# Kernel tuning notes

Measured on AMD Instinct MI355X. Metric: run time of the kernel, lower is better.

Reference implementation:

```python
import jax, jax.numpy as jnp
import numpy as np

N = 50000      # nodes
E = 800000     # random edges (self-loops added in reference, per PyG GATConv default)
F_IN = 128
B = 512        # graphs in the batch
NEG_SLOPE = 0.2  # PyG GATConv leaky_relu default


def setup_inputs() -> dict:
    key = jax.random.key(0)
    ks = jax.random.split(key, 12)
    def w(k, shape, fan_in):
        return jax.random.normal(k, shape, jnp.float32) / np.sqrt(fan_in)
    return {
        "x": jax.random.normal(ks[0], (N, F_IN), jnp.float32),
        "edge_index": jax.random.randint(ks[1], (2, E), 0, N, dtype=jnp.int32),
        "batch": jnp.sort(jax.random.randint(ks[2], (N,), 0, B, dtype=jnp.int32)),
        "W1": w(ks[3], (F_IN, 4 * 64), F_IN),
        "a_src1": w(ks[4], (4, 64), 64),
        "a_dst1": w(ks[5], (4, 64), 64),
        "b1": jnp.zeros((4 * 64,), jnp.float32),
        "W2": w(ks[6], (256, 1 * 128), 256),
        "a_src2": w(ks[7], (1, 128), 128),
        "a_dst2": w(ks[8], (1, 128), 128),
        "b2": jnp.zeros((128,), jnp.float32),
        "Wl": w(ks[9], (128, 1), 128),
        "bl": jnp.zeros((1,), jnp.float32),
    }


def gat_layer(x, src, dst, W, a_src, a_dst, b, n):
    H, Fo = a_src.shape
    h = (x @ W).reshape(n, H, Fo)                      # [N,H,Fo]
    alpha_s = jnp.einsum("nhf,hf->nh", h, a_src)       # [N,H]
    alpha_d = jnp.einsum("nhf,hf->nh", h, a_dst)
    e = jax.nn.leaky_relu(alpha_s[src] + alpha_d[dst], NEG_SLOPE)  # [E,H]
    # segment softmax over incoming edges of each dst node
    m = jax.ops.segment_max(e, dst, num_segments=n)    # [N,H]; self-loops => every node hit
    ex = jnp.exp(e - m[dst])
    den = jax.ops.segment_sum(ex, dst, num_segments=n)
    alpha = ex / den[dst]                              # [E,H]
    out = jax.ops.segment_sum(h[src] * alpha[:, :, None], dst, num_segments=n)
    return out.reshape(n, H * Fo) + b


def reference(x, edge_index, batch, W1, a_src1, a_dst1, b1, W2, a_src2, a_dst2, b2, Wl, bl):
    n = x.shape[0]
    loops = jnp.arange(n, dtype=edge_index.dtype)
    src = jnp.concatenate([edge_index[0], loops])
    dst = jnp.concatenate([edge_index[1], loops])
    h = jax.nn.elu(gat_layer(x, src, dst, W1, a_src1, a_dst1, b1, n))
    h = jax.nn.elu(gat_layer(h, src, dst, W2, a_src2, a_dst2, b2, n))
    # dropout omitted (inference)
    sums = jax.ops.segment_sum(h, batch, num_segments=B)
    cnt = jax.ops.segment_sum(jnp.ones((n,), h.dtype), batch, num_segments=B)
    g = sums / jnp.maximum(cnt, 1.0)[:, None]          # global_mean_pool -> [B,128]
    return jax.nn.sigmoid(g @ Wl + bl).reshape(-1)     # [B]
```

## Files before the change

### kernel.cpp

```cpp
#include <hip/hip_runtime.h>
#include <hip/hip_bf16.h>

#define NN 50000
#define EE 800000
#define ETOT 850000
#define BB 512
#define CAP 64
#define SCAT_BLKS ((ETOT + 255) / 256)

typedef __hip_bfloat16 bf16;
typedef __attribute__((ext_vector_type(8))) __bf16 v8bf;
typedef __attribute__((ext_vector_type(4))) float f32x4;

__device__ __forceinline__ float lo2f(unsigned int u) {
    return __uint_as_float(u << 16);
}
__device__ __forceinline__ float hi2f(unsigned int u) {
    return __uint_as_float(u & 0xffff0000u);
}
__device__ __forceinline__ float us2f(unsigned short u) {
    return __uint_as_float(((unsigned int)u) << 16);
}
__device__ __forceinline__ unsigned short f2bfbits(float f) {
    bf16 h = __float2bfloat16(f);
    return *reinterpret_cast<unsigned short*>(&h);
}
__device__ __forceinline__ float lrelu_exp(float ev) {
    ev = ev > 0.f ? ev : 0.2f * ev;
    return __expf(fminf(ev, 80.f));
}

__global__ void k_prep(const float* __restrict__ W1, const float* __restrict__ W2,
                       bf16* __restrict__ wt1, bf16* __restrict__ wt2,
                       int* __restrict__ deg, float* __restrict__ gsum) {
    int idx = blockIdx.x * blockDim.x + threadIdx.x;
    if (idx < 256 * 128) {
        int c = idx >> 7, k = idx & 127;
        wt1[idx] = __float2bfloat16(W1[k * 256 + c]);
    } else {
        int j = idx - 256 * 128;
        int c = j >> 8, k = j & 255;
        wt2[j] = __float2bfloat16(W2[k * 128 + c]);
    }
    if (idx < NN) deg[idx] = 0;
    gsum[idx] = 0.f;
}

__global__ __launch_bounds__(256, 2)
void k_scatter_gemm1(const int* __restrict__ srcArr, const int* __restrict__ dstArr,
                     int* __restrict__ deg, unsigned short* __restrict__ csrc,
                     const float* __restrict__ x, const bf16* __restrict__ wt1,
                     const float* __restrict__ aw_s, const float* __restrict__ aw_d,
                     bf16* __restrict__ h1, float* __restrict__ as1,
                     float* __restrict__ ad1) {
    __shared__ bf16 xs[32 * 136];
    if (blockIdx.x < SCAT_BLKS) {
        int e = blockIdx.x * 256 + threadIdx.x;
        if (e < ETOT) {
            int d, s;
            if (e < EE) { d = dstArr[e]; s = srcArr[e]; }
            else        { d = e - EE;    s = d; }
            d = min(max(d, 0), NN - 1);
            s = min(max(s, 0), NN - 1);
            int p = atomicAdd(&deg[d], 1);
            if (p < CAP) csrc[d * CAP + p] = (unsigned short)s;
        }
        return;
    }

    int bid = blockIdx.x - SCAT_BLKS;
    int n0 = bid * 32;
    int t = threadIdx.x;
    for (int i = 0; i < 4; i++) {
        int idx = t + 256 * i;
        int r = idx >> 5, c4 = idx & 31;
        float4 v = make_float4(0.f, 0.f, 0.f, 0.f);
        if (n0 + r < NN) v = *(const float4*)(x + (size_t)(n0 + r) * 128 + c4 * 4);
        ushort4 o;
        o.x = f2bfbits(v.x); o.y = f2bfbits(v.y);
        o.z = f2bfbits(v.z); o.w = f2bfbits(v.w);
        *(ushort4*)(&xs[r * 136 + c4 * 4]) = o;
    }
    __syncthreads();

    int wv = t >> 6, lane = t & 63;
    int q = lane >> 4, r16 = lane & 15;
    int rowBase = (wv & 1) * 16;
    int colBase = (wv >> 1) * 128;

    f32x4 acc[8];
#pragma unroll
    for (int ct = 0; ct < 8; ct++) acc[ct] = (f32x4){0.f, 0.f, 0.f, 0.f};

#pragma unroll
    for (int kt = 0; kt < 4; kt++) {
        v8bf va = *(const v8bf*)(&xs[(rowBase + r16) * 136 + kt * 32 + q * 8]);
#pragma unroll
        for (int ct = 0; ct < 8; ct++) {
            v8bf vb = *(const v8bf*)(wt1 + (size_t)(colBase + ct * 16 + r16) * 128 + kt * 32 + q * 8);
            acc[ct] = __builtin_amdgcn_mfma_f32_16x16x32_bf16(va, vb, acc[ct], 0, 0, 0);
        }
    }

    float wsv[8], wdv[8];
#pragma unroll
    for (int ct = 0; ct < 8; ct++) {
        int col = colBase + ct * 16 + r16;
        wsv[ct] = aw_s[col];
        wdv[ct] = aw_d[col];
    }

    float ps[4][2], pd[4][2];
#pragma unroll
    for (int reg = 0; reg < 4; reg++) {
        ps[reg][0] = 0.f; ps[reg][1] = 0.f;
        pd[reg][0] = 0.f; pd[reg][1] = 0.f;
    }

#pragma unroll
    for (int reg = 0; reg < 4; reg++) {
        int node = n0 + rowBase + q * 4 + reg;
        bool ok = node < NN;
#pragma unroll
        for (int ct = 0; ct < 8; ct++) {
            float v = acc[ct][reg];
            if (ok) h1[(size_t)node * 256 + colBase + ct * 16 + r16] = __float2bfloat16(v);
            ps[reg][ct >> 2] += v * wsv[ct];
            pd[reg][ct >> 2] += v * wdv[ct];
        }
    }

#pragma unroll
    for (int reg = 0; reg < 4; reg++) {
        int node = n0 + rowBase + q * 4 + reg;
        bool ok = node < NN;
#pragma unroll
        for (int lh = 0; lh < 2; lh++) {
            float a = ps[reg][lh], b = pd[reg][lh];
            for (int mask = 1; mask <= 8; mask <<= 1) {
                a += __shfl_xor(a, mask);
                b += __shfl_xor(b, mask);
            }
            if (r16 == 0 && ok) {
                int head = (wv >> 1) * 2 + lh;
                as1[node * 4 + head] = a;
                ad1[node * 4 + head] = b;
            }
        }
    }
}

__global__ void k_gather1(const unsigned short* __restrict__ csrc, const int* __restrict__ deg,
                          const bf16* __restrict__ h1, const float* __restrict__ as1,
                          const float* __restrict__ ad1, const float* __restrict__ b1,
                          bf16* __restrict__ x2) {
    int bid = blockIdx.x;
    int n = bid >> 1, slice = bid & 1;
    int t = threadIdx.x;
    int lh = t >> 5;
    int cnt = min(deg[n], CAP);
    float2 ad = *(const float2*)&ad1[n * 4 + slice * 2];
    __shared__ unsigned int ls[CAP];
    __shared__ float la[CAP * 2];
    const char* h1c = (const char*)h1;
    unsigned int tconst = (unsigned int)(slice * 128 + t * 2) * 2;
    if (t < cnt) {
        int s = (int)csrc[n * CAP + t];
        ls[t] = (unsigned int)s << 9;
        float2 as = *(const float2*)&as1[s * 4 + slice * 2];
        la[t * 2 + 0] = lrelu_exp(as.x + ad.x);
        la[t * 2 + 1] = lrelu_exp(as.y + ad.y);
    }
    __syncthreads();
    float a0 = 0.f, a1 = 0.f, ssum = 0.f;
    int j = 0;
    for (; j + 3 < cnt; j += 4) {
        unsigned int o0 = ls[j] + tconst, o1 = ls[j + 1] + tconst;
        unsigned int o2 = ls[j + 2] + tconst, o3 = ls[j + 3] + tconst;
        float A0 = la[j * 2 + lh], A1 = la[j * 2 + 2 + lh];
        float A2 = la[j * 2 + 4 + lh], A3 = la[j * 2 + 6 + lh];
        unsigned int u0 = *(const unsigned int*)(h1c + o0);
        unsigned int u1 = *(const unsigned int*)(h1c + o1);
        unsigned int u2 = *(const unsigned int*)(h1c + o2);
        unsigned int u3 = *(const unsigned int*)(h1c + o3);
        ssum += (A0 + A1) + (A2 + A3);
        a0 = fmaf(A0, lo2f(u0), a0); a0 = fmaf(A1, lo2f(u1), a0);
        a0 = fmaf(A2, lo2f(u2), a0); a0 = fmaf(A3, lo2f(u3), a0);
        a1 = fmaf(A0, hi2f(u0), a1); a1 = fmaf(A1, hi2f(u1), a1);
        a1 = fmaf(A2, hi2f(u2), a1); a1 = fmaf(A3, hi2f(u3), a1);
    }
    for (; j < cnt; j++) {
        unsigned int o0 = ls[j] + tconst;
        float A0 = la[j * 2 + lh];
        unsigned int u0 = *(const unsigned int*)(h1c + o0);
        ssum += A0;
        a0 = fmaf(A0, lo2f(u0), a0);
        a1 = fmaf(A0, hi2f(u0), a1);
    }
    float inv = 1.f / fmaxf(ssum, 1e-35f);
    int c = slice * 128 + t * 2;
    float r0 = a0 * inv + b1[c + 0];
    float r1 = a1 * inv + b1[c + 1];
    r0 = r0 > 0.f ? r0 : (__expf(r0) - 1.f);
    r1 = r1 > 0.f ? r1 : (__expf(r1) - 1.f);
    unsigned int packed = (unsigned int)f2bfbits(r0) | ((unsigned int)f2bfbits(r1) << 16);
    *(unsigned int*)((unsigned short*)x2 + (size_t)n * 256 + c) = packed;
}

__global__ __launch_bounds__(256, 2)
void k_gemm2(const bf16* __restrict__ x2, const bf16* __restrict__ wt2,
             const float* __restrict__ aw_s, const float* __restrict__ aw_d,
             bf16* __restrict__ h2, float* __restrict__ as2,
             float* __restrict__ ad2) {
    int n0 = blockIdx.x * 32;
    int t = threadIdx.x;
    __shared__ bf16 xs[32 * 264];
    __shared__ float psPart[32][2];
    __shared__ float pdPart[32][2];
    for (int i = 0; i < 4; i++) {
        int idx = t + 256 * i;
        int r = idx >> 5, c8 = idx & 31;
        uint4 v;
        if (n0 + r < NN) v = *(const uint4*)(x2 + (size_t)(n0 + r) * 256 + c8 * 8);
        else             v = make_uint4(0, 0, 0, 0);
        *(uint4*)(&xs[r * 264 + c8 * 8]) = v;
    }
    __syncthreads();

    int wv = t >> 6, lane = t & 63;
    int q = lane >> 4, r16 = lane & 15;
    int rowBase = (wv & 1) * 16;
    int colBase = (wv >> 1) * 64;

    f32x4 acc[4];
#pragma unroll
    for (int ct = 0; ct < 4; ct++) acc[ct] = (f32x4){0.f, 0.f, 0.f, 0.f};

#pragma unroll
    for (int kt = 0; kt < 8; kt++) {
        v8bf va = *(const v8bf*)(&xs[(rowBase + r16) * 264 + kt * 32 + q * 8]);
#pragma unroll
        for (int ct = 0; ct < 4; ct++) {
            v8bf vb = *(const v8bf*)(wt2 + (size_t)(colBase + ct * 16 + r16) * 256 + kt * 32 + q * 8);
            acc[ct] = __builtin_amdgcn_mfma_f32_16x16x32_bf16(va, vb, acc[ct], 0, 0, 0);
        }
    }

    float wsv[4], wdv[4];
#pragma unroll
    for (int ct = 0; ct < 4; ct++) {
        int col = colBase + ct * 16 + r16;
        wsv[ct] = aw_s[col];
        wdv[ct] = aw_d[col];
    }

#pragma unroll
    for (int reg = 0; reg < 4; reg++) {
        int node = n0 + rowBase + q * 4 + reg;
        bool ok = node < NN;
        float ps = 0.f, pd = 0.f;
#pragma unroll
        for (int ct = 0; ct < 4; ct++) {
            float v = acc[ct][reg];
            if (ok) h2[(size_t)node * 128 + colBase + ct * 16 + r16] = __float2bfloat16(v);
            ps += v * wsv[ct];
            pd += v * wdv[ct];
        }
        for (int mask = 1; mask <= 8; mask <<= 1) {
            ps += __shfl_xor(ps, mask);
            pd += __shfl_xor(pd, mask);
        }
        if (r16 == 0) {
            int li = rowBase + q * 4 + reg;
            psPart[li][wv >> 1] = ps;
            pdPart[li][wv >> 1] = pd;
        }
    }
    __syncthreads();
    if (t < 32) {
        int node = n0 + t;
        if (node < NN) {
            as2[node] = psPart[t][0] + psPart[t][1];
            ad2[node] = pdPart[t][0] + pdPart[t][1];
        }
    }
}

__global__ __launch_bounds__(512, 2)
void k_gather2pool(const unsigned short* __restrict__ csrc, const int* __restrict__ deg,
                   const bf16* __restrict__ h2, const float* __restrict__ as2,
                   const float* __restrict__ ad2, const float* __restrict__ b2,
                   const int* __restrict__ batch, float* __restrict__ gsum) {
    int wv = threadIdx.x >> 6;
    int t = threadIdx.x & 63;
    int n = blockIdx.x * 8 + wv;
    int cnt = min(deg[n], CAP);
    float adn = ad2[n];
    __shared__ unsigned int ls[8][CAP];
    __shared__ float la[8][CAP];
    __shared__ float acc[8][128];
    const char* h2c = (const char*)h2;
    unsigned int tconst = (unsigned int)t * 4;
    if (t < cnt) {
        int s = (int)csrc[n * CAP + t];
        ls[wv][t] = (unsigned int)s << 8;
        la[wv][t] = lrelu_exp(as2[s] + adn);
    }
    __syncthreads();
    const unsigned int* lsw = ls[wv];
    const float* law = la[wv];
    float a0 = 0.f, a1 = 0.f, ssum = 0.f;
    int j = 0;
    for (; j + 3 < cnt; j += 4) {
        unsigned int o0 = lsw[j] + tconst, o1 = lsw[j + 1] + tconst;
        unsigned int o2 = lsw[j + 2] + tconst, o3 = lsw[j + 3] + tconst;
        float A0 = law[j], A1 = law[j + 1], A2 = law[j + 2], A3 = law[j + 3];
        unsigned int u0 = *(const unsigned int*)(h2c + o0);
        unsigned int u1 = *(const unsigned int*)(h2c + o1);
        unsigned int u2 = *(const unsigned int*)(h2c + o2);
        unsigned int u3 = *(const unsigned int*)(h2c + o3);
        ssum += (A0 + A1) + (A2 + A3);
        a0 = fmaf(A0, lo2f(u0), a0); a0 = fmaf(A1, lo2f(u1), a0);
        a0 = fmaf(A2, lo2f(u2), a0); a0 = fmaf(A3, lo2f(u3), a0);
        a1 = fmaf(A0, hi2f(u0), a1); a1 = fmaf(A1, hi2f(u1), a1);
        a1 = fmaf(A2, hi2f(u2), a1); a1 = fmaf(A3, hi2f(u3), a1);
    }
    for (; j < cnt; j++) {
        unsigned int o0 = lsw[j] + tconst;
        float A0 = law[j];
        unsigned int u0 = *(const unsigned int*)(h2c + o0);
        ssum += A0;
        a0 = fmaf(A0, lo2f(u0), a0);
        a1 = fmaf(A0, hi2f(u0), a1);
    }
    float inv = 1.f / fmaxf(ssum, 1e-35f);
    int c = t * 2;
    float r0 = a0 * inv + b2[c + 0];
    float r1 = a1 * inv + b2[c + 1];
    r0 = r0 > 0.f ? r0 : (__expf(r0) - 1.f);
    r1 = r1 > 0.f ? r1 : (__expf(r1) - 1.f);
    acc[wv][c] = r0;
    acc[wv][c + 1] = r1;
    __syncthreads();
    int tt = threadIdx.x;
    if (tt < 128) {
        int n0 = blockIdx.x * 8;
        int b0 = batch[n0], b7 = batch[n0 + 7];
        if (b0 == b7) {
            float s = 0.f;
#pragma unroll
            for (int w = 0; w < 8; w++) s += acc[w][tt];
            atomicAdd(&gsum[b0 * 128 + tt], s);
        } else {
#pragma unroll
            for (int w = 0; w < 8; w++)
                atomicAdd(&gsum[batch[n0 + w] * 128 + tt], acc[w][tt]);
        }
    }
}

__global__ void k_out(const float* __restrict__ gsum, const int* __restrict__ batch,
                      const float* __restrict__ Wl, const float* __restrict__ bl,
                      float* __restrict__ out) {
    int b = blockIdx.x;
    int t = threadIdx.x;
    int lo = 0, hi = NN;
    while (lo < hi) { int m = (lo + hi) >> 1; if (batch[m] < b) lo = m + 1; else hi = m; }
    int start = lo;
    int lo2 = start, hi2 = NN;
    while (lo2 < hi2) { int m = (lo2 + hi2) >> 1; if (batch[m] < b + 1) lo2 = m + 1; else hi2 = m; }
    int cnt = lo2 - start;
    float g = gsum[b * 128 + t] / (float)(cnt > 0 ? cnt : 1);
    float p = g * Wl[t];
    for (int o = 32; o > 0; o >>= 1) p += __shfl_down(p, o);
    __shared__ float red[2];
    if ((t & 63) == 0) red[t >> 6] = p;
    __syncthreads();
    if (t == 0) {
        float acc = red[0] + red[1] + bl[0];
        out[b] = 1.f / (1.f + __expf(-acc));
    }
}

extern "C" void kernel_launch(void* const* d_in, const int* in_sizes, int n_in,
                              void* d_out, int out_size, void* d_ws, size_t ws_size,
                              hipStream_t stream) {
    const float* x = (const float*)d_in[0];
    const int* ei = (const int*)d_in[1];
    const int* batch = (const int*)d_in[2];
    const float* W1 = (const float*)d_in[3];
    const float* aw_s1 = (const float*)d_in[4];
    const float* aw_d1 = (const float*)d_in[5];
    const float* b1 = (const float*)d_in[6];
    const float* W2 = (const float*)d_in[7];
    const float* aw_s2 = (const float*)d_in[8];
    const float* aw_d2 = (const float*)d_in[9];
    const float* b2 = (const float*)d_in[10];
    const float* Wl = (const float*)d_in[11];
    const float* bl = (const float*)d_in[12];
    const int* srcArr = ei;
    const int* dstArr = ei + EE;

    char* w = (char*)d_ws;
    size_t off = 0;
    auto alloc = [&](size_t bytes) -> void* {
        void* p = (void*)(w + off);
        off = (off + bytes + 255) & ~(size_t)255;
        return p;
    };
    bf16* bufA = (bf16*)alloc((size_t)NN * 256 * 2);
    bf16* bufB = (bf16*)alloc((size_t)NN * 256 * 2);
    unsigned short* csrc = (unsigned short*)alloc((size_t)NN * CAP * 2);
    float* as1 = (float*)alloc((size_t)NN * 4 * 4);
    float* ad1 = (float*)alloc((size_t)NN * 4 * 4);
    float* as2 = (float*)alloc((size_t)NN * 4);
    float* ad2 = (float*)alloc((size_t)NN * 4);
    int* deg = (int*)alloc((size_t)NN * 4);
    float* gsum = (float*)alloc((size_t)BB * 128 * 4);
    bf16* wt1 = (bf16*)alloc((size_t)256 * 128 * 2);
    bf16* wt2 = (bf16*)alloc((size_t)128 * 256 * 2);
    (void)ws_size;

    k_prep<<<256, 256, 0, stream>>>(W1, W2, wt1, wt2, deg, gsum);

    bf16* h1 = bufA;
    bf16* x2 = bufB;
    int gemmBlocks = (NN + 31) / 32;
    k_scatter_gemm1<<<SCAT_BLKS + gemmBlocks, 256, 0, stream>>>(
        srcArr, dstArr, deg, csrc, x, wt1, aw_s1, aw_d1, h1, as1, ad1);

    k_gather1<<<NN * 2, 64, 0, stream>>>(csrc, deg, h1, as1, ad1, b1, x2);

    bf16* h2 = bufA;
    k_gemm2<<<gemmBlocks, 256, 0, stream>>>(x2, wt2, aw_s2, aw_d2, h2, as2, ad2);

    k_gather2pool<<<NN / 8, 512, 0, stream>>>(csrc, deg, h2, as2, ad2, b2, batch, gsum);

    k_out<<<BB, 128, 0, stream>>>(gsum, batch, Wl, bl, (float*)d_out);
}
```

Baseline: 310.0 us.

## Build compact CSR adjacency via count, scan and place instead of padded slots

Replaces the fixed-capacity padded per-node neighbor table with a compact CSR layout. The first kernel now only counts in-degrees, with self-loops seeded by initialising the counts to one. A single-block scan then computes offsets and places each node's self-loop, and a placement kernel scatters the edge sources through atomic cursors. The gather kernels read contiguous neighbor lists, shrinking the adjacency footprint, at the cost of two extra launches and a serial single-block scan.

```diff
diff --git a/kernel.cpp b/kernel.cpp
--- a/kernel.cpp
+++ b/kernel.cpp
@@ -3,14 +3,14 @@
 
 #define NN 50000
 #define EE 800000
-#define ETOT 850000
 #define BB 512
 #define CAP 64
-#define SCAT_BLKS ((ETOT + 255) / 256)
 
 typedef __hip_bfloat16 bf16;
 typedef __attribute__((ext_vector_type(8))) __bf16 v8bf;
 typedef __attribute__((ext_vector_type(4))) float f32x4;
+
+#define CNT_BLKS ((EE + 255) / 256)
 
 __device__ __forceinline__ float lo2f(unsigned int u) {
     return __uint_as_float(u << 16);
@@ -42,33 +42,29 @@
         int c = j >> 8, k = j & 255;
         wt2[j] = __float2bfloat16(W2[k * 128 + c]);
     }
-    if (idx < NN) deg[idx] = 0;
+    if (idx < NN) deg[idx] = 1;
     gsum[idx] = 0.f;
 }
 
 __global__ __launch_bounds__(256, 2)
-void k_scatter_gemm1(const int* __restrict__ srcArr, const int* __restrict__ dstArr,
-                     int* __restrict__ deg, unsigned short* __restrict__ csrc,
-                     const float* __restrict__ x, const bf16* __restrict__ wt1,
-                     const float* __restrict__ aw_s, const float* __restrict__ aw_d,
-                     bf16* __restrict__ h1, float* __restrict__ as1,
-                     float* __restrict__ ad1) {
+void k_count_gemm1(const int* __restrict__ dstArr,
+                   int* __restrict__ deg,
+                   const float* __restrict__ x, const bf16* __restrict__ wt1,
+                   const float* __restrict__ aw_s, const float* __restrict__ aw_d,
+                   bf16* __restrict__ h1, float* __restrict__ as1,
+                   float* __restrict__ ad1) {
     __shared__ bf16 xs[32 * 136];
-    if (blockIdx.x < SCAT_BLKS) {
+    if (blockIdx.x < CNT_BLKS) {
         int e = blockIdx.x * 256 + threadIdx.x;
-        if (e < ETOT) {
-            int d, s;
-            if (e < EE) { d = dstArr[e]; s = srcArr[e]; }
-            else        { d = e - EE;    s = d; }
+        if (e < EE) {
+            int d = dstArr[e];
             d = min(max(d, 0), NN - 1);
-            s = min(max(s, 0), NN - 1);
-            int p = atomicAdd(&deg[d], 1);
-            if (p < CAP) csrc[d * CAP + p] = (unsigned short)s;
+            atomicAdd(&deg[d], 1);
         }
         return;
     }
 
-    int bid = blockIdx.x - SCAT_BLKS;
+    int bid = blockIdx.x - CNT_BLKS;
     int n0 = bid * 32;
     int t = threadIdx.x;
     for (int i = 0; i < 4; i++) {
@@ -150,7 +146,43 @@
     }
 }
 
-__global__ void k_gather1(const unsigned short* __restrict__ csrc, const int* __restrict__ deg,
+__global__ __launch_bounds__(1024)
+void k_scan(const int* __restrict__ deg, int* __restrict__ cursor,
+            unsigned short* __restrict__ adj) {
+    __shared__ int partial[1024];
+    int t = threadIdx.x;
+    int lo = t * 49, hi = min(lo + 49, NN);
+    int s = 0;
+    for (int i = lo; i < hi; i++) s += deg[i];
+    partial[t] = s;
+    __syncthreads();
+    for (int off = 1; off < 1024; off <<= 1) {
+        int add = (t >= off) ? partial[t - off] : 0;
+        __syncthreads();
+        partial[t] += add;
+        __syncthreads();
+    }
+    int base = partial[t] - s;
+    for (int i = lo; i < hi; i++) {
+        adj[base] = (unsigned short)i;
+        cursor[i] = base + 1;
+        base += deg[i];
+    }
+}
+
+__global__ void k_place(const int* __restrict__ srcArr, const int* __restrict__ dstArr,
+                        int* __restrict__ cursor, unsigned short* __restrict__ adj) {
+    int e = blockIdx.x * 256 + threadIdx.x;
+    if (e >= EE) return;
+    int d = dstArr[e], s = srcArr[e];
+    d = min(max(d, 0), NN - 1);
+    s = min(max(s, 0), NN - 1);
+    int p = atomicAdd(&cursor[d], 1);
+    adj[p] = (unsigned short)s;
+}
+
+__global__ void k_gather1(const unsigned short* __restrict__ adj, const int* __restrict__ deg,
+                          const int* __restrict__ cursor,
                           const bf16* __restrict__ h1, const float* __restrict__ as1,
                           const float* __restrict__ ad1, const float* __restrict__ b1,
                           bf16* __restrict__ x2) {
@@ -158,14 +190,16 @@
     int n = bid >> 1, slice = bid & 1;
     int t = threadIdx.x;
     int lh = t >> 5;
-    int cnt = min(deg[n], CAP);
+    int dn = deg[n];
+    int cnt = min(dn, CAP);
+    int base = cursor[n] - dn;
     float2 ad = *(const float2*)&ad1[n * 4 + slice * 2];
     __shared__ unsigned int ls[CAP];
     __shared__ float la[CAP * 2];
     const char* h1c = (const char*)h1;
     unsigned int tconst = (unsigned int)(slice * 128 + t * 2) * 2;
     if (t < cnt) {
-        int s = (int)csrc[n * CAP + t];
+        int s = (int)adj[base + t];
         ls[t] = (unsigned int)s << 9;
         float2 as = *(const float2*)&as1[s * 4 + slice * 2];
         la[t * 2 + 0] = lrelu_exp(as.x + ad.x);
@@ -287,14 +321,17 @@
 }
 
 __global__ __launch_bounds__(512, 2)
-void k_gather2pool(const unsigned short* __restrict__ csrc, const int* __restrict__ deg,
+void k_gather2pool(const unsigned short* __restrict__ adj, const int* __restrict__ deg,
+                   const int* __restrict__ cursor,
                    const bf16* __restrict__ h2, const float* __restrict__ as2,
                    const float* __restrict__ ad2, const float* __restrict__ b2,
                    const int* __restrict__ batch, float* __restrict__ gsum) {
     int wv = threadIdx.x >> 6;
     int t = threadIdx.x & 63;
     int n = blockIdx.x * 8 + wv;
-    int cnt = min(deg[n], CAP);
+    int dn = deg[n];
+    int cnt = min(dn, CAP);
+    int base = cursor[n] - dn;
     float adn = ad2[n];
     __shared__ unsigned int ls[8][CAP];
     __shared__ float la[8][CAP];
@@ -302,7 +339,7 @@
     const char* h2c = (const char*)h2;
     unsigned int tconst = (unsigned int)t * 4;
     if (t < cnt) {
-        int s = (int)csrc[n * CAP + t];
+        int s = (int)adj[base + t];
         ls[wv][t] = (unsigned int)s << 8;
         la[wv][t] = lrelu_exp(as2[s] + adn);
     }
@@ -410,7 +447,8 @@
     };
     bf16* bufA = (bf16*)alloc((size_t)NN * 256 * 2);
     bf16* bufB = (bf16*)alloc((size_t)NN * 256 * 2);
-    unsigned short* csrc = (unsigned short*)alloc((size_t)NN * CAP * 2);
+    unsigned short* adj = (unsigned short*)alloc((size_t)(EE + NN) * 2);
+    int* cursor = (int*)alloc((size_t)NN * 4);
     float* as1 = (float*)alloc((size_t)NN * 4 * 4);
     float* ad1 = (float*)alloc((size_t)NN * 4 * 4);
     float* as2 = (float*)alloc((size_t)NN * 4);
@@ -426,15 +464,18 @@
     bf16* h1 = bufA;
     bf16* x2 = bufB;
     int gemmBlocks = (NN + 31) / 32;
-    k_scatter_gemm1<<<SCAT_BLKS + gemmBlocks, 256, 0, stream>>>(
-        srcArr, dstArr, deg, csrc, x, wt1, aw_s1, aw_d1, h1, as1, ad1);
-
-    k_gather1<<<NN * 2, 64, 0, stream>>>(csrc, deg, h1, as1, ad1, b1, x2);
+    k_count_gemm1<<<CNT_BLKS + gemmBlocks, 256, 0, stream>>>(
+        dstArr, deg, x, wt1, aw_s1, aw_d1, h1, as1, ad1);
+
+    k_scan<<<1, 1024, 0, stream>>>(deg, cursor, adj);
+    k_place<<<CNT_BLKS, 256, 0, stream>>>(srcArr, dstArr, cursor, adj);
+
+    k_gather1<<<NN * 2, 64, 0, stream>>>(adj, deg, cursor, h1, as1, ad1, b1, x2);
 
     bf16* h2 = bufA;
     k_gemm2<<<gemmBlocks, 256, 0, stream>>>(x2, wt2, aw_s2, aw_d2, h2, as2, ad2);
 
-    k_gather2pool<<<NN / 8, 512, 0, stream>>>(csrc, deg, h2, as2, ad2, b2, batch, gsum);
+    k_gather2pool<<<NN / 8, 512, 0, stream>>>(adj, deg, cursor, h2, as2, ad2, b2, batch, gsum);
 
     k_out<<<BB, 128, 0, stream>>>(gsum, batch, Wl, bl, (float*)d_out);
 }
```

Result: slower. 445.0 us (+43.6%).

## Fuse layer-1 attention aggregation into the layer-2 GEMM kernel

Applied to the files above, without the earlier changes.

Removes the separate layer-1 gather kernel. Each wave of the GEMM2 block now aggregates 8 destination nodes across all 4 heads directly into the shared-memory tile that feeds the MFMA, instead of writing the intermediate x2 to global memory and reading it back. The gather loop now uses 8-byte loads per lane covering 4 columns, and vector LDS reads of indices and weights, unrolled by 8. This avoids a full write and read of the intermediate activation and one kernel launch. The cost is coarser parallelism, since each block holds 32 nodes with uneven degrees, plus heavier per-block work and LDS use under a new occupancy hint.

```diff
diff --git a/kernel.cpp b/kernel.cpp
--- a/kernel.cpp
+++ b/kernel.cpp
@@ -150,85 +150,121 @@
     }
 }
 
-__global__ void k_gather1(const unsigned short* __restrict__ csrc, const int* __restrict__ deg,
-                          const bf16* __restrict__ h1, const float* __restrict__ as1,
-                          const float* __restrict__ ad1, const float* __restrict__ b1,
-                          bf16* __restrict__ x2) {
-    int bid = blockIdx.x;
-    int n = bid >> 1, slice = bid & 1;
-    int t = threadIdx.x;
-    int lh = t >> 5;
-    int cnt = min(deg[n], CAP);
-    float2 ad = *(const float2*)&ad1[n * 4 + slice * 2];
-    __shared__ unsigned int ls[CAP];
-    __shared__ float la[CAP * 2];
-    const char* h1c = (const char*)h1;
-    unsigned int tconst = (unsigned int)(slice * 128 + t * 2) * 2;
-    if (t < cnt) {
-        int s = (int)csrc[n * CAP + t];
-        ls[t] = (unsigned int)s << 9;
-        float2 as = *(const float2*)&as1[s * 4 + slice * 2];
-        la[t * 2 + 0] = lrelu_exp(as.x + ad.x);
-        la[t * 2 + 1] = lrelu_exp(as.y + ad.y);
-    }
-    __syncthreads();
-    float a0 = 0.f, a1 = 0.f, ssum = 0.f;
-    int j = 0;
-    for (; j + 3 < cnt; j += 4) {
-        unsigned int o0 = ls[j] + tconst, o1 = ls[j + 1] + tconst;
-        unsigned int o2 = ls[j + 2] + tconst, o3 = ls[j + 3] + tconst;
-        float A0 = la[j * 2 + lh], A1 = la[j * 2 + 2 + lh];
-        float A2 = la[j * 2 + 4 + lh], A3 = la[j * 2 + 6 + lh];
-        unsigned int u0 = *(const unsigned int*)(h1c + o0);
-        unsigned int u1 = *(const unsigned int*)(h1c + o1);
-        unsigned int u2 = *(const unsigned int*)(h1c + o2);
-        unsigned int u3 = *(const unsigned int*)(h1c + o3);
-        ssum += (A0 + A1) + (A2 + A3);
-        a0 = fmaf(A0, lo2f(u0), a0); a0 = fmaf(A1, lo2f(u1), a0);
-        a0 = fmaf(A2, lo2f(u2), a0); a0 = fmaf(A3, lo2f(u3), a0);
-        a1 = fmaf(A0, hi2f(u0), a1); a1 = fmaf(A1, hi2f(u1), a1);
-        a1 = fmaf(A2, hi2f(u2), a1); a1 = fmaf(A3, hi2f(u3), a1);
-    }
-    for (; j < cnt; j++) {
-        unsigned int o0 = ls[j] + tconst;
-        float A0 = la[j * 2 + lh];
-        unsigned int u0 = *(const unsigned int*)(h1c + o0);
-        ssum += A0;
-        a0 = fmaf(A0, lo2f(u0), a0);
-        a1 = fmaf(A0, hi2f(u0), a1);
-    }
-    float inv = 1.f / fmaxf(ssum, 1e-35f);
-    int c = slice * 128 + t * 2;
-    float r0 = a0 * inv + b1[c + 0];
-    float r1 = a1 * inv + b1[c + 1];
-    r0 = r0 > 0.f ? r0 : (__expf(r0) - 1.f);
-    r1 = r1 > 0.f ? r1 : (__expf(r1) - 1.f);
-    unsigned int packed = (unsigned int)f2bfbits(r0) | ((unsigned int)f2bfbits(r1) << 16);
-    *(unsigned int*)((unsigned short*)x2 + (size_t)n * 256 + c) = packed;
-}
-
-__global__ __launch_bounds__(256, 2)
-void k_gemm2(const bf16* __restrict__ x2, const bf16* __restrict__ wt2,
-             const float* __restrict__ aw_s, const float* __restrict__ aw_d,
-             bf16* __restrict__ h2, float* __restrict__ as2,
-             float* __restrict__ ad2) {
+__global__ __launch_bounds__(256, 4)
+void k_agg_gemm2(const unsigned short* __restrict__ csrc, const int* __restrict__ deg,
+                 const bf16* __restrict__ h1, const float* __restrict__ as1,
+                 const float* __restrict__ ad1, const float* __restrict__ b1,
+                 const bf16* __restrict__ wt2, const float* __restrict__ aw_s,
+                 const float* __restrict__ aw_d, bf16* __restrict__ h2,
+                 float* __restrict__ as2, float* __restrict__ ad2) {
     int n0 = blockIdx.x * 32;
     int t = threadIdx.x;
+    int wv = t >> 6, l = t & 63;
     __shared__ bf16 xs[32 * 264];
     __shared__ float psPart[32][2];
     __shared__ float pdPart[32][2];
-    for (int i = 0; i < 4; i++) {
-        int idx = t + 256 * i;
-        int r = idx >> 5, c8 = idx & 31;
-        uint4 v;
-        if (n0 + r < NN) v = *(const uint4*)(x2 + (size_t)(n0 + r) * 256 + c8 * 8);
-        else             v = make_uint4(0, 0, 0, 0);
-        *(uint4*)(&xs[r * 264 + c8 * 8]) = v;
-    }
-    __syncthreads();
-
-    int wv = t >> 6, lane = t & 63;
-    int q = lane >> 4, r16 = lane & 15;
+    __shared__ unsigned int lsb[4][CAP];
+    __shared__ float lab[4][4 * 68];
+
+    const char* h1c = (const char*)h1;
+    const unsigned int* lsw = lsb[wv];
+    const float* lah = &lab[wv][(l >> 4) * 68];
+    unsigned int tconst = (unsigned int)l * 8;
+
+    for (int k = 0; k < 8; k++) {
+        int n = n0 + wv * 8 + k;
+        bool okn = n < NN;
+        int cnt = okn ? min(deg[n], CAP) : 0;
+        if (l < cnt) {
+            int s = (int)csrc[n * CAP + l];
+            lsb[wv][l] = (unsigned int)s << 9;
+            float4 as = *(const float4*)&as1[s * 4];
+            float4 ad = *(const float4*)&ad1[n * 4];
+            lab[wv][0 * 68 + l] = lrelu_exp(as.x + ad.x);
+            lab[wv][1 * 68 + l] = lrelu_exp(as.y + ad.y);
+            lab[wv][2 * 68 + l] = lrelu_exp(as.z + ad.z);
+            lab[wv][3 * 68 + l] = lrelu_exp(as.w + ad.w);
+        }
+        float a0 = 0.f, a1 = 0.f, a2 = 0.f, a3 = 0.f, ssum = 0.f;
+        int j = 0;
+        for (; j + 7 < cnt; j += 8) {
+            uint4 ov0 = *(const uint4*)&lsw[j];
+            uint4 ov1 = *(const uint4*)&lsw[j + 4];
+            float4 A0 = *(const float4*)&lah[j];
+            float4 A1 = *(const float4*)&lah[j + 4];
+            uint2 d0 = *(const uint2*)(h1c + (ov0.x + tconst));
+            uint2 d1 = *(const uint2*)(h1c + (ov0.y + tconst));
+            uint2 d2 = *(const uint2*)(h1c + (ov0.z + tconst));
+            uint2 d3 = *(const uint2*)(h1c + (ov0.w + tconst));
+            uint2 d4 = *(const uint2*)(h1c + (ov1.x + tconst));
+            uint2 d5 = *(const uint2*)(h1c + (ov1.y + tconst));
+            uint2 d6 = *(const uint2*)(h1c + (ov1.z + tconst));
+            uint2 d7 = *(const uint2*)(h1c + (ov1.w + tconst));
+            ssum += (A0.x + A0.y) + (A0.z + A0.w) + (A1.x + A1.y) + (A1.z + A1.w);
+            a0 = fmaf(A0.x, lo2f(d0.x), a0); a1 = fmaf(A0.x, hi2f(d0.x), a1);
+            a2 = fmaf(A0.x, lo2f(d0.y), a2); a3 = fmaf(A0.x, hi2f(d0.y), a3);
+            a0 = fmaf(A0.y, lo2f(d1.x), a0); a1 = fmaf(A0.y, hi2f(d1.x), a1);
+            a2 = fmaf(A0.y, lo2f(d1.y), a2); a3 = fmaf(A0.y, hi2f(d1.y), a3);
+            a0 = fmaf(A0.z, lo2f(d2.x), a0); a1 = fmaf(A0.z, hi2f(d2.x), a1);
+            a2 = fmaf(A0.z, lo2f(d2.y), a2); a3 = fmaf(A0.z, hi2f(d2.y), a3);
+            a0 = fmaf(A0.w, lo2f(d3.x), a0); a1 = fmaf(A0.w, hi2f(d3.x), a1);
+            a2 = fmaf(A0.w, lo2f(d3.y), a2); a3 = fmaf(A0.w, hi2f(d3.y), a3);
+            a0 = fmaf(A1.x, lo2f(d4.x), a0); a1 = fmaf(A1.x, hi2f(d4.x), a1);
+            a2 = fmaf(A1.x, lo2f(d4.y), a2); a3 = fmaf(A1.x, hi2f(d4.y), a3);
+            a0 = fmaf(A1.y, lo2f(d5.x), a0); a1 = fmaf(A1.y, hi2f(d5.x), a1);
+            a2 = fmaf(A1.y, lo2f(d5.y), a2); a3 = fmaf(A1.y, hi2f(d5.y), a3);
+            a0 = fmaf(A1.z, lo2f(d6.x), a0); a1 = fmaf(A1.z, hi2f(d6.x), a1);
+            a2 = fmaf(A1.z, lo2f(d6.y), a2); a3 = fmaf(A1.z, hi2f(d6.y), a3);
+            a0 = fmaf(A1.w, lo2f(d7.x), a0); a1 = fmaf(A1.w, hi2f(d7.x), a1);
+            a2 = fmaf(A1.w, lo2f(d7.y), a2); a3 = fmaf(A1.w, hi2f(d7.y), a3);
+        }
+        for (; j + 3 < cnt; j += 4) {
+            uint4 ov0 = *(const uint4*)&lsw[j];
+            float4 A0 = *(const float4*)&lah[j];
+            uint2 d0 = *(const uint2*)(h1c + (ov0.x + tconst));
+            uint2 d1 = *(const uint2*)(h1c + (ov0.y + tconst));
+            uint2 d2 = *(const uint2*)(h1c + (ov0.z + tconst));
+            uint2 d3 = *(const uint2*)(h1c + (ov0.w + tconst));
+            ssum += (A0.x + A0.y) + (A0.z + A0.w);
+            a0 = fmaf(A0.x, lo2f(d0.x), a0); a1 = fmaf(A0.x, hi2f(d0.x), a1);
+            a2 = fmaf(A0.x, lo2f(d0.y), a2); a3 = fmaf(A0.x, hi2f(d0.y), a3);
+            a0 = fmaf(A0.y, lo2f(d1.x), a0); a1 = fmaf(A0.y, hi2f(d1.x), a1);
+            a2 = fmaf(A0.y, lo2f(d1.y), a2); a3 = fmaf(A0.y, hi2f(d1.y), a3);
+            a0 = fmaf(A0.z, lo2f(d2.x), a0); a1 = fmaf(A0.z, hi2f(d2.x), a1);
+            a2 = fmaf(A0.z, lo2f(d2.y), a2); a3 = fmaf(A0.z, hi2f(d2.y), a3);
+            a0 = fmaf(A0.w, lo2f(d3.x), a0); a1 = fmaf(A0.w, hi2f(d3.x), a1);
+            a2 = fmaf(A0.w, lo2f(d3.y), a2); a3 = fmaf(A0.w, hi2f(d3.y), a3);
+        }
+        for (; j < cnt; j++) {
+            unsigned int o0 = lsw[j] + tconst;
+            float A0 = lah[j];
+            uint2 d0 = *(const uint2*)(h1c + o0);
+            ssum += A0;
+            a0 = fmaf(A0, lo2f(d0.x), a0); a1 = fmaf(A0, hi2f(d0.x), a1);
+            a2 = fmaf(A0, lo2f(d0.y), a2); a3 = fmaf(A0, hi2f(d0.y), a3);
+        }
+        int row = wv * 8 + k;
+        int c = l * 4;
+        uint2 packed = make_uint2(0u, 0u);
+        if (okn) {
+            float inv = 1.f / fmaxf(ssum, 1e-35f);
+            float4 bv = *(const float4*)&b1[c];
+            float r0 = a0 * inv + bv.x;
+            float r1 = a1 * inv + bv.y;
+            float r2 = a2 * inv + bv.z;
+            float r3 = a3 * inv + bv.w;
+            r0 = r0 > 0.f ? r0 : (__expf(r0) - 1.f);
+            r1 = r1 > 0.f ? r1 : (__expf(r1) - 1.f);
+            r2 = r2 > 0.f ? r2 : (__expf(r2) - 1.f);
+            r3 = r3 > 0.f ? r3 : (__expf(r3) - 1.f);
+            packed.x = (unsigned int)f2bfbits(r0) | ((unsigned int)f2bfbits(r1) << 16);
+            packed.y = (unsigned int)f2bfbits(r2) | ((unsigned int)f2bfbits(r3) << 16);
+        }
+        *(uint2*)(&xs[row * 264 + c]) = packed;
+    }
+    __syncthreads();
+
+    int q = l >> 4, r16 = l & 15;
     int rowBase = (wv & 1) * 16;
     int colBase = (wv >> 1) * 64;
 
@@ -408,8 +444,8 @@
         off = (off + bytes + 255) & ~(size_t)255;
         return p;
     };
-    bf16* bufA = (bf16*)alloc((size_t)NN * 256 * 2);
-    bf16* bufB = (bf16*)alloc((size_t)NN * 256 * 2);
+    bf16* h1 = (bf16*)alloc((size_t)NN * 256 * 2);
+    bf16* h2 = (bf16*)alloc((size_t)NN * 128 * 2);
     unsigned short* csrc = (unsigned short*)alloc((size_t)NN * CAP * 2);
     float* as1 = (float*)alloc((size_t)NN * 4 * 4);
     float* ad1 = (float*)alloc((size_t)NN * 4 * 4);
@@ -423,16 +459,12 @@
 
     k_prep<<<256, 256, 0, stream>>>(W1, W2, wt1, wt2, deg, gsum);
 
-    bf16* h1 = bufA;
-    bf16* x2 = bufB;
     int gemmBlocks = (NN + 31) / 32;
     k_scatter_gemm1<<<SCAT_BLKS + gemmBlocks, 256, 0, stream>>>(
         srcArr, dstArr, deg, csrc, x, wt1, aw_s1, aw_d1, h1, as1, ad1);
 
-    k_gather1<<<NN * 2, 64, 0, stream>>>(csrc, deg, h1, as1, ad1, b1, x2);
-
-    bf16* h2 = bufA;
-    k_gemm2<<<gemmBlocks, 256, 0, stream>>>(x2, wt2, aw_s2, aw_d2, h2, as2, ad2);
+    k_agg_gemm2<<<gemmBlocks, 256, 0, stream>>>(
+        csrc, deg, h1, as1, ad1, b1, wt2, aw_s2, aw_d2, h2, as2, ad2);
 
     k_gather2pool<<<NN / 8, 512, 0, stream>>>(csrc, deg, h2, as2, ad2, b2, batch, gsum);
 
```

Measured after the change: 305.2 us. No clear change (-1.5%).
